# Performance work log

Measured on AMD Instinct MI355X. Metric: run time of the kernel, lower is better.

## Reference

```python
import jax, jax.numpy as jnp
import numpy as np
import math

B, S, D = 4, 2048, 1024
H = 1
HD = D // H  # head_dim == hidden_dim since num_heads=1 (required by source's phase_encoder Linear)
HALF = HD // 2
SYNC_LOSS_WEIGHT = 0.01


def setup_inputs() -> dict:
    key = jax.random.key(0)
    ks = jax.random.split(key, 11)
    wstd = 0.02
    inp = {
        "x": jax.random.normal(ks[0], (B, S, D), dtype=jnp.float32),
        "Wq": jax.random.normal(ks[1], (D, D), dtype=jnp.float32) * wstd,
        "bq": jnp.zeros((D,), jnp.float32),
        "Wk": jax.random.normal(ks[2], (D, D), dtype=jnp.float32) * wstd,
        "bk": jnp.zeros((D,), jnp.float32),
        "Wv": jax.random.normal(ks[3], (D, D), dtype=jnp.float32) * wstd,
        "bv": jnp.zeros((D,), jnp.float32),
        "Wp": jax.random.normal(ks[4], (D, D), dtype=jnp.float32) * wstd,
        "bp": jnp.zeros((D,), jnp.float32),
        "Wo": jax.random.normal(ks[5], (D, D), dtype=jnp.float32) * wstd,
        "bo": jnp.zeros((D,), jnp.float32),
        "bifurcation_param": jnp.asarray(1.0, jnp.float32),
        "phase_coupling": jnp.asarray(0.5, jnp.float32),
    }
    return inp


def _phase(t, Wp, bp):
    # t: [B,H,S,HD] -> instantaneous phase via angle(complex(first_half, second_half))
    pf = t @ Wp.T + bp
    re, im = pf[..., :HALF], pf[..., HALF:]
    return jnp.arctan2(im, re)  # [B,H,S,HALF]


def reference(x, Wq, bq, Wk, bk, Wv, bv, Wp, bp, Wo, bo, bifurcation_param, phase_coupling):
    b, s, d = x.shape
    Q = (x @ Wq.T + bq).reshape(b, s, H, HD).transpose(0, 2, 1, 3)  # [B,H,S,HD]
    K = (x @ Wk.T + bk).reshape(b, s, H, HD).transpose(0, 2, 1, 3)
    V = (x @ Wv.T + bv).reshape(b, s, H, HD).transpose(0, 2, 1, 3)

    scores = jnp.einsum("bhqd,bhkd->bhqk", Q, K) / math.sqrt(HD)

    pQ = _phase(Q, Wp, bp)
    pK = _phase(K, Wp, bp)
    # mean_d cos(pQ - pK) == (cos(pQ)@cos(pK)^T + sin(pQ)@sin(pK)^T) / HALF
    sync = (jnp.einsum("bhqd,bhkd->bhqk", jnp.cos(pQ), jnp.cos(pK))
            + jnp.einsum("bhqd,bhkd->bhqk", jnp.sin(pQ), jnp.sin(pK))) / HALF

    t = jnp.tanh(scores)
    bif = bifurcation_param * t * (1.0 - t)

    chaotic = scores + phase_coupling * sync + bif
    attn = jax.nn.softmax(chaotic, axis=-1)

    av = jnp.einsum("bhqk,bhkd->bhqd", attn, V)
    av = av.transpose(0, 2, 1, 3).reshape(b, s, d)
    out = av @ Wo.T + bo

    # torch.var default: unbiased (ddof=1), over last dim of sync
    sync_loss = SYNC_LOSS_WEIGHT * jnp.var(sync, axis=-1, ddof=1).mean()
    return out, sync_loss
```

## Files before the change

kernel.cpp:

```cpp
#include <hip/hip_runtime.h>
#include <hip/hip_bf16.h>
#include <math.h>

#define S_LEN 2048
#define D_MODEL 1024
#define N_BATCH 4
#define N_HALF 512

typedef unsigned short u16;
typedef __attribute__((ext_vector_type(8))) short bf16x8;
typedef __attribute__((ext_vector_type(4))) float f32x4;

__device__ inline u16 f2bf(float v) {
  __hip_bfloat16 h = __float2bfloat16(v);
  return *reinterpret_cast<u16*>(&h);
}
__device__ inline float bf2f(u16 u) {
  __hip_bfloat16 h = *reinterpret_cast<__hip_bfloat16*>(&u);
  return __bfloat162float(h);
}
__device__ inline void gl2lds16(const void* g, void* l) {
  __builtin_amdgcn_global_load_lds(
      (const __attribute__((address_space(1))) unsigned int*)g,
      (__attribute__((address_space(3))) unsigned int*)l, 16, 0, 0);
}
__device__ inline float fast_tanh(float x) {
  float e = __expf(2.0f * x);
  return 1.0f - 2.0f / (e + 1.0f);
}

__global__ __launch_bounds__(256)
void cast_bf4(const float* __restrict__ src, u16* __restrict__ dst, long long n4) {
  long long i = (long long)blockIdx.x * 256 + threadIdx.x;
  if (i >= n4) return;
  float4 v = ((const float4*)src)[i];
  ushort4 o;
  o.x = f2bf(v.x); o.y = f2bf(v.y); o.z = f2bf(v.z); o.w = f2bf(v.w);
  ((ushort4*)dst)[i] = o;
}
__global__ __launch_bounds__(256)
void cast_split(const float* __restrict__ src, u16* __restrict__ hi,
                u16* __restrict__ lo, long long n) {
  long long i = (long long)blockIdx.x * 256 + threadIdx.x;
  if (i < n) {
    float v = src[i];
    u16 h = f2bf(v);
    hi[i] = h;
    lo[i] = f2bf(v - bf2f(h));
  }
}
__global__ __launch_bounds__(256)
void transpose_split(const float* __restrict__ src, u16* __restrict__ hi,
                     u16* __restrict__ lo) {
  __shared__ float t[32][33];
  const int bx = blockIdx.x * 32;
  const int by = blockIdx.y * 32;
  const int c = threadIdx.x & 31;
  const int r0 = (threadIdx.x >> 5) * 4;
#pragma unroll
  for (int r = 0; r < 4; r++)
    t[r0 + r][c] = src[(long long)(by + r0 + r) * D_MODEL + bx + c];
  __syncthreads();
#pragma unroll
  for (int r = 0; r < 4; r++) {
    float v = t[c][r0 + r];
    long long idx = (long long)(bx + r0 + r) * D_MODEL + by + c;
    u16 h = f2bf(v);
    hi[idx] = h;
    lo[idx] = f2bf(v - bf2f(h));
  }
}
__global__ __launch_bounds__(256)
void zero_stats(float* __restrict__ p, int n) {
  int i = blockIdx.x * 256 + threadIdx.x;
  if (i < n) p[i] = 0.f;
}
__global__ __launch_bounds__(256)
void w2_bias(const float* __restrict__ Wo, const float* __restrict__ bv,
             float* __restrict__ w2b) {
  const int d = blockIdx.x;
  const int tid = threadIdx.x;
  float acc = 0.f;
  for (int j = tid; j < D_MODEL; j += 256)
    acc += Wo[(long long)d * D_MODEL + j] * bv[j];
#pragma unroll
  for (int m = 1; m < 64; m <<= 1) acc += __shfl_xor(acc, m);
  __shared__ float red[4];
  if ((tid & 63) == 0) red[tid >> 6] = acc;
  __syncthreads();
  if (tid == 0) w2b[d] = red[0] + red[1] + red[2] + red[3];
}


__global__ __launch_bounds__(256, 2)
void qk_fused(const u16* __restrict__ X, const u16* __restrict__ Wq,
              const u16* __restrict__ Wk,
              const float* __restrict__ bq, const float* __restrict__ bk,
              u16* __restrict__ Qo, u16* __restrict__ Ko) {
  __shared__ u16 Xs[128 * 64];
  __shared__ u16 Qs[128 * 64];
  __shared__ u16 Ks[128 * 64];
  const int tid  = threadIdx.x;
  const int wave = tid >> 6;
  const int lane = tid & 63;
  const int quad = lane >> 4;
  const int tc   = lane & 15;
  const int bm = blockIdx.y * 128;
  const int bn = blockIdx.x * 128;
  const int wm = (wave & 1) * 64;
  const int wn = (wave >> 1) * 64;

  f32x4 acc1[4][4], acc2[4][4];
#pragma unroll
  for (int i = 0; i < 4; i++)
#pragma unroll
    for (int j = 0; j < 4; j++) {
      acc1[i][j] = (f32x4){0.f, 0.f, 0.f, 0.f};
      acc2[i][j] = (f32x4){0.f, 0.f, 0.f, 0.f};
    }

  const int srow8 = lane >> 3;
  const int scol  = ((lane & 7) ^ srow8) * 8;
  const int srowb = wave * 32;
  const u16* gx = X  + (long long)(bm + srowb + srow8) * D_MODEL + scol;
  const u16* gq = Wq + (long long)(bn + srowb + srow8) * D_MODEL + scol;
  const u16* gk = Wk + (long long)(bn + srowb + srow8) * D_MODEL + scol;
  const int wb = srowb * 64;
  const long long r8 = 8LL * D_MODEL;
  const int swzA = tc & 7;

  for (int k0 = 0; k0 < D_MODEL; k0 += 64) {
#pragma unroll
    for (int c = 0; c < 4; c++) {
      gl2lds16(gx + c * r8, Xs + wb + c * 512);
      gl2lds16(gq + c * r8, Qs + wb + c * 512);
      gl2lds16(gk + c * r8, Ks + wb + c * 512);
    }
    gx += 64; gq += 64; gk += 64;
    __syncthreads();
    bf16x8 af[4][2], bq4[4][2], bk4[4][2];
#pragma unroll
    for (int i = 0; i < 4; i++) {
      const int ra = (wm + i * 16 + tc) * 64;
      const int rb = (wn + i * 16 + tc) * 64;
#pragma unroll
      for (int ks = 0; ks < 2; ks++) {
        const int co = ((ks * 4 + quad) ^ swzA) * 8;
        af[i][ks]  = *(const bf16x8*)(Xs + ra + co);
        bq4[i][ks] = *(const bf16x8*)(Qs + rb + co);
        bk4[i][ks] = *(const bf16x8*)(Ks + rb + co);
      }
    }
#pragma unroll
    for (int i = 0; i < 4; i++)
#pragma unroll
      for (int j = 0; j < 4; j++) {
        acc1[i][j] = __builtin_amdgcn_mfma_f32_16x16x32_bf16(af[i][0], bq4[j][0], acc1[i][j], 0, 0, 0);
        acc2[i][j] = __builtin_amdgcn_mfma_f32_16x16x32_bf16(af[i][0], bk4[j][0], acc2[i][j], 0, 0, 0);
        acc1[i][j] = __builtin_amdgcn_mfma_f32_16x16x32_bf16(af[i][1], bq4[j][1], acc1[i][j], 0, 0, 0);
        acc2[i][j] = __builtin_amdgcn_mfma_f32_16x16x32_bf16(af[i][1], bk4[j][1], acc2[i][j], 0, 0, 0);
      }
    __syncthreads();
  }

#pragma unroll
  for (int i = 0; i < 4; i++) {
    const int row0 = bm + wm + i * 16 + quad * 4;
#pragma unroll
    for (int j = 0; j < 4; j++) {
      const int col = bn + wn + j * 16 + tc;
#pragma unroll
      for (int r = 0; r < 4; r++) {
        long long idx = (long long)(row0 + r) * D_MODEL + col;
        Qo[idx] = f2bf(acc1[i][j][r] + bq[col]);
        Ko[idx] = f2bf(acc2[i][j][r] + bk[col]);
      }
    }
  }
}

__global__ __launch_bounds__(256, 2)
void pf_fused(const u16* __restrict__ Qb, const u16* __restrict__ Wp,
              const float* __restrict__ bp,
              u16* __restrict__ pfQ, u16* __restrict__ pfK,
              long long TDo) {
  __shared__ u16 Qs[128 * 64];
  __shared__ u16 Ks[128 * 64];
  __shared__ u16 Ws[128 * 64];
  const int tid  = threadIdx.x;
  const int wave = tid >> 6;
  const int lane = tid & 63;
  const int quad = lane >> 4;
  const int tc   = lane & 15;
  const int bm = blockIdx.y * 128;
  const int bn = blockIdx.x * 128;
  const int wm = (wave & 1) * 64;
  const int wn = (wave >> 1) * 64;

  f32x4 acc1[4][4], acc2[4][4];
#pragma unroll
  for (int i = 0; i < 4; i++)
#pragma unroll
    for (int j = 0; j < 4; j++) {
      acc1[i][j] = (f32x4){0.f, 0.f, 0.f, 0.f};
      acc2[i][j] = (f32x4){0.f, 0.f, 0.f, 0.f};
    }

  const int srow8 = lane >> 3;
  const int scol  = ((lane & 7) ^ srow8) * 8;
  const int srowb = wave * 32;
  const u16* gq = Qb + (long long)(bm + srowb + srow8) * D_MODEL + scol;
  const u16* gk = gq + TDo;
  const u16* gw = Wp + (long long)(bn + srowb + srow8) * D_MODEL + scol;
  const int wb = srowb * 64;
  const long long r8 = 8LL * D_MODEL;
  const int swzA = tc & 7;

  for (int k0 = 0; k0 < D_MODEL; k0 += 64) {
#pragma unroll
    for (int c = 0; c < 4; c++) {
      gl2lds16(gq + c * r8, Qs + wb + c * 512);
      gl2lds16(gk + c * r8, Ks + wb + c * 512);
      gl2lds16(gw + c * r8, Ws + wb + c * 512);
    }
    gq += 64; gk += 64; gw += 64;
    __syncthreads();
    bf16x8 aq[4][2], ak[4][2], bw[4][2];
#pragma unroll
    for (int i = 0; i < 4; i++) {
      const int ra = (wm + i * 16 + tc) * 64;
      const int rb = (wn + i * 16 + tc) * 64;
#pragma unroll
      for (int ks = 0; ks < 2; ks++) {
        const int co = ((ks * 4 + quad) ^ swzA) * 8;
        aq[i][ks] = *(const bf16x8*)(Qs + ra + co);
        ak[i][ks] = *(const bf16x8*)(Ks + ra + co);
        bw[i][ks] = *(const bf16x8*)(Ws + rb + co);
      }
    }
#pragma unroll
    for (int i = 0; i < 4; i++)
#pragma unroll
      for (int j = 0; j < 4; j++) {
        acc1[i][j] = __builtin_amdgcn_mfma_f32_16x16x32_bf16(aq[i][0], bw[j][0], acc1[i][j], 0, 0, 0);
        acc2[i][j] = __builtin_amdgcn_mfma_f32_16x16x32_bf16(ak[i][0], bw[j][0], acc2[i][j], 0, 0, 0);
        acc1[i][j] = __builtin_amdgcn_mfma_f32_16x16x32_bf16(aq[i][1], bw[j][1], acc1[i][j], 0, 0, 0);
        acc2[i][j] = __builtin_amdgcn_mfma_f32_16x16x32_bf16(ak[i][1], bw[j][1], acc2[i][j], 0, 0, 0);
      }
    __syncthreads();
  }

#pragma unroll
  for (int i = 0; i < 4; i++) {
    const int row0 = bm + wm + i * 16 + quad * 4;
#pragma unroll
    for (int j = 0; j < 4; j++) {
      const int col = bn + wn + j * 16 + tc;
#pragma unroll
      for (int r = 0; r < 4; r++) {
        long long idx = (long long)(row0 + r) * D_MODEL + col;
        float b = bp[col];
        pfQ[idx] = f2bf(acc1[i][j][r] + b);
        pfK[idx] = f2bf(acc2[i][j][r] + b);
      }
    }
  }
}

__global__ __launch_bounds__(256)
void mfma_gemm_out3(const u16* __restrict__ Ah, const u16* __restrict__ Al,
                    const u16* __restrict__ Bh, const u16* __restrict__ Bl,
                    const float* __restrict__ bias, float* __restrict__ C,
                    int N, int K) {
  __shared__ u16 Ash[128 * 64];
  __shared__ u16 Asl[128 * 64];
  __shared__ u16 Bsh[128 * 64];
  __shared__ u16 Bsl[128 * 64];
  const int tid  = threadIdx.x;
  const int wave = tid >> 6;
  const int lane = tid & 63;
  const int quad = lane >> 4;
  const int tc   = lane & 15;
  const int bm = blockIdx.y * 128;
  const int bn = blockIdx.x * 128;
  const int wm = (wave & 1) * 64;
  const int wn = (wave >> 1) * 64;

  f32x4 acc[4][4];
#pragma unroll
  for (int i = 0; i < 4; i++)
#pragma unroll
    for (int j = 0; j < 4; j++) acc[i][j] = (f32x4){0.f, 0.f, 0.f, 0.f};

  const int srow8 = lane >> 3;
  const int scol  = ((lane & 7) ^ srow8) * 8;
  const int srowb = wave * 32;
  long long aoff = (long long)(bm + srowb + srow8) * K + scol;
  long long boff = (long long)(bn + srowb + srow8) * K + scol;
  const u16 *gah = Ah + aoff, *gal = Al + aoff;
  const u16 *gbh = Bh + boff, *gbl = Bl + boff;
  const int wb = srowb * 64;
  const long long r8K = 8LL * K;
  const int swzA = tc & 7;

  for (int k0 = 0; k0 < K; k0 += 64) {
#pragma unroll
    for (int c = 0; c < 4; c++) {
      gl2lds16(gah + c * r8K, Ash + wb + c * 512);
      gl2lds16(gal + c * r8K, Asl + wb + c * 512);
      gl2lds16(gbh + c * r8K, Bsh + wb + c * 512);
      gl2lds16(gbl + c * r8K, Bsl + wb + c * 512);
    }
    gah += 64; gal += 64; gbh += 64; gbl += 64;
    __syncthreads();
    bf16x8 ah[4][2], al[4][2], bh[4][2], bl[4][2];
#pragma unroll
    for (int i = 0; i < 4; i++) {
      const int ra = (wm + i * 16 + tc) * 64;
      const int rb = (wn + i * 16 + tc) * 64;
#pragma unroll
      for (int ks = 0; ks < 2; ks++) {
        const int co = ((ks * 4 + quad) ^ swzA) * 8;
        ah[i][ks] = *(const bf16x8*)(Ash + ra + co);
        al[i][ks] = *(const bf16x8*)(Asl + ra + co);
        bh[i][ks] = *(const bf16x8*)(Bsh + rb + co);
        bl[i][ks] = *(const bf16x8*)(Bsl + rb + co);
      }
    }
#pragma unroll
    for (int i = 0; i < 4; i++)
#pragma unroll
      for (int j = 0; j < 4; j++) {
#pragma unroll
        for (int ks = 0; ks < 2; ks++) {
          acc[i][j] = __builtin_amdgcn_mfma_f32_16x16x32_bf16(ah[i][ks], bh[j][ks], acc[i][j], 0, 0, 0);
          acc[i][j] = __builtin_amdgcn_mfma_f32_16x16x32_bf16(ah[i][ks], bl[j][ks], acc[i][j], 0, 0, 0);
          acc[i][j] = __builtin_amdgcn_mfma_f32_16x16x32_bf16(al[i][ks], bh[j][ks], acc[i][j], 0, 0, 0);
        }
      }
    __syncthreads();
  }
#pragma unroll
  for (int i = 0; i < 4; i++) {
    const int row0 = bm + wm + i * 16 + quad * 4;
#pragma unroll
    for (int j = 0; j < 4; j++) {
      const int col = bn + wn + j * 16 + tc;
      float b = bias ? bias[col] : 0.f;
#pragma unroll
      for (int r = 0; r < 4; r++)
        C[(long long)(row0 + r) * N + col] = acc[i][j][r] + b;
    }
  }
}

__global__ __launch_bounds__(256)
void vwt_kernel(const u16* __restrict__ W2h, const u16* __restrict__ W2l,
                const u16* __restrict__ X, const float* __restrict__ w2b,
                u16* __restrict__ Ch, u16* __restrict__ Cl,
                long long sB, long long sC) {
  __shared__ u16 Ah[128 * 64];
  __shared__ u16 Al[128 * 64];
  __shared__ u16 Bs[128 * 64];
  const int tid  = threadIdx.x;
  const int wave = tid >> 6;
  const int lane = tid & 63;
  const int quad = lane >> 4;
  const int tc   = lane & 15;
  const int bm = blockIdx.y * 128;
  const int bn = blockIdx.x * 128;
  const long long z = blockIdx.z;
  const int wm = (wave & 1) * 64;
  const int wn = (wave >> 1) * 64;

  f32x4 acc[4][4];
#pragma unroll
  for (int i = 0; i < 4; i++)
#pragma unroll
    for (int j = 0; j < 4; j++) acc[i][j] = (f32x4){0.f, 0.f, 0.f, 0.f};

  const int srow8 = lane >> 3;
  const int scol  = ((lane & 7) ^ srow8) * 8;
  const int srowb = wave * 32;
  const long long aoff = (long long)(bm + srowb + srow8) * D_MODEL + scol;
  const u16* gah = W2h + aoff;
  const u16* gal = W2l + aoff;
  const u16* gb  = X + z * sB + (long long)(bn + srowb + srow8) * D_MODEL + scol;
  const int wb = srowb * 64;
  const long long r8 = 8LL * D_MODEL;
  const int swzA = tc & 7;

  for (int k0 = 0; k0 < D_MODEL; k0 += 64) {
#pragma unroll
    for (int c = 0; c < 4; c++) {
      gl2lds16(gah + c * r8, Ah + wb + c * 512);
      gl2lds16(gal + c * r8, Al + wb + c * 512);
      gl2lds16(gb  + c * r8, Bs + wb + c * 512);
    }
    gah += 64; gal += 64; gb += 64;
    __syncthreads();
    bf16x8 ah4[4][2], al4[4][2], bx[4][2];
#pragma unroll
    for (int i = 0; i < 4; i++) {
      const int ra = (wm + i * 16 + tc) * 64;
      const int rb = (wn + i * 16 + tc) * 64;
#pragma unroll
      for (int ks = 0; ks < 2; ks++) {
        const int co = ((ks * 4 + quad) ^ swzA) * 8;
        ah4[i][ks] = *(const bf16x8*)(Ah + ra + co);
        al4[i][ks] = *(const bf16x8*)(Al + ra + co);
        bx[i][ks]  = *(const bf16x8*)(Bs + rb + co);
      }
    }
#pragma unroll
    for (int i = 0; i < 4; i++)
#pragma unroll
      for (int j = 0; j < 4; j++) {
        acc[i][j] = __builtin_amdgcn_mfma_f32_16x16x32_bf16(ah4[i][0], bx[j][0], acc[i][j], 0, 0, 0);
        acc[i][j] = __builtin_amdgcn_mfma_f32_16x16x32_bf16(al4[i][0], bx[j][0], acc[i][j], 0, 0, 0);
        acc[i][j] = __builtin_amdgcn_mfma_f32_16x16x32_bf16(ah4[i][1], bx[j][1], acc[i][j], 0, 0, 0);
        acc[i][j] = __builtin_amdgcn_mfma_f32_16x16x32_bf16(al4[i][1], bx[j][1], acc[i][j], 0, 0, 0);
      }
    __syncthreads();
  }

  u16* Chz = Ch + z * sC;
  u16* Clz = Cl + z * sC;
#pragma unroll
  for (int i = 0; i < 4; i++) {
    const int row0 = bm + wm + i * 16 + quad * 4;
#pragma unroll
    for (int j = 0; j < 4; j++) {
      const int col = bn + wn + j * 16 + tc;
#pragma unroll
      for (int r = 0; r < 4; r++) {
        float v = acc[i][j][r] + w2b[row0 + r];
        long long idx = (long long)(row0 + r) * S_LEN + col;
        u16 h = f2bf(v);
        Chz[idx] = h;
        Clz[idx] = f2bf(v - bf2f(h));
      }
    }
  }
}

__global__ __launch_bounds__(256)
void gemm_bsplit(const u16* __restrict__ A,
                 const u16* __restrict__ Bh, const u16* __restrict__ Bl,
                 const float* __restrict__ bias, float* __restrict__ C,
                 int N, int K, long long sA, long long sB, long long sC) {
  __shared__ u16 As[128 * 64];
  __shared__ u16 Bsh[128 * 64];
  __shared__ u16 Bsl[128 * 64];
  const int tid  = threadIdx.x;
  const int wave = tid >> 6;
  const int lane = tid & 63;
  const int quad = lane >> 4;
  const int tc   = lane & 15;
  const int bm = blockIdx.y * 128;
  const int bn = blockIdx.x * 128;
  const long long z = blockIdx.z;
  const int wm = (wave & 1) * 64;
  const int wn = (wave >> 1) * 64;

  f32x4 acc[4][4];
#pragma unroll
  for (int i = 0; i < 4; i++)
#pragma unroll
    for (int j = 0; j < 4; j++) acc[i][j] = (f32x4){0.f, 0.f, 0.f, 0.f};

  const int srow8 = lane >> 3;
  const int scol  = ((lane & 7) ^ srow8) * 8;
  const int srowb = wave * 32;
  const long long boff = (long long)(bn + srowb + srow8) * K + scol;
  const u16* ga  = A + z * sA + (long long)(bm + srowb + srow8) * K + scol;
  const u16* gbh = Bh + z * sB + boff;
  const u16* gbl = Bl + z * sB + boff;
  const int wb = srowb * 64;
  const long long r8K = 8LL * K;
  const int swzA = tc & 7;

  for (int k0 = 0; k0 < K; k0 += 64) {
#pragma unroll
    for (int c = 0; c < 4; c++) {
      gl2lds16(ga  + c * r8K, As  + wb + c * 512);
      gl2lds16(gbh + c * r8K, Bsh + wb + c * 512);
      gl2lds16(gbl + c * r8K, Bsl + wb + c * 512);
    }
    ga += 64; gbh += 64; gbl += 64;
    __syncthreads();
    bf16x8 af[4][2], bh[4][2], bl[4][2];
#pragma unroll
    for (int i = 0; i < 4; i++) {
      const int ra = (wm + i * 16 + tc) * 64;
      const int rb = (wn + i * 16 + tc) * 64;
#pragma unroll
      for (int ks = 0; ks < 2; ks++) {
        const int co = ((ks * 4 + quad) ^ swzA) * 8;
        af[i][ks] = *(const bf16x8*)(As  + ra + co);
        bh[i][ks] = *(const bf16x8*)(Bsh + rb + co);
        bl[i][ks] = *(const bf16x8*)(Bsl + rb + co);
      }
    }
#pragma unroll
    for (int i = 0; i < 4; i++)
#pragma unroll
      for (int j = 0; j < 4; j++) {
        acc[i][j] = __builtin_amdgcn_mfma_f32_16x16x32_bf16(af[i][0], bh[j][0], acc[i][j], 0, 0, 0);
        acc[i][j] = __builtin_amdgcn_mfma_f32_16x16x32_bf16(af[i][0], bl[j][0], acc[i][j], 0, 0, 0);
        acc[i][j] = __builtin_amdgcn_mfma_f32_16x16x32_bf16(af[i][1], bh[j][1], acc[i][j], 0, 0, 0);
        acc[i][j] = __builtin_amdgcn_mfma_f32_16x16x32_bf16(af[i][1], bl[j][1], acc[i][j], 0, 0, 0);
      }
    __syncthreads();
  }

  float* Cz = C + z * sC;
#pragma unroll
  for (int i = 0; i < 4; i++) {
    const int row0 = bm + wm + i * 16 + quad * 4;
#pragma unroll
    for (int j = 0; j < 4; j++) {
      const int col = bn + wn + j * 16 + tc;
#pragma unroll
      for (int r = 0; r < 4; r++)
        Cz[(long long)(row0 + r) * N + col] = acc[i][j][r] + bias[col];
    }
  }
}

__global__ __launch_bounds__(256, 2)
void chaotic_fused(const u16* __restrict__ Q, const u16* __restrict__ Kt,
                   const u16* __restrict__ Uq, const u16* __restrict__ Uk,
                   float* __restrict__ Cc,
                   float* __restrict__ ssum, float* __restrict__ ssq,
                   const float* __restrict__ bifp, const float* __restrict__ pcp) {
  __shared__ u16 Qs[128 * 64];
  __shared__ u16 Ks[128 * 64];
  __shared__ u16 Us[128 * 64];
  __shared__ u16 Ws[128 * 64];
  const int tid  = threadIdx.x;
  const int wave = tid >> 6;
  const int lane = tid & 63;
  const int quad = lane >> 4;
  const int tc   = lane & 15;
  const int bm = blockIdx.y * 128;
  const int bn = blockIdx.x * 128;
  const long long z = blockIdx.z;
  const long long sQ = (long long)S_LEN * D_MODEL;
  const int wm = (wave & 1) * 64;
  const int wn = (wave >> 1) * 64;

  f32x4 acc1[4][4], acc2[4][4];
#pragma unroll
  for (int i = 0; i < 4; i++)
#pragma unroll
    for (int j = 0; j < 4; j++) {
      acc1[i][j] = (f32x4){0.f, 0.f, 0.f, 0.f};
      acc2[i][j] = (f32x4){0.f, 0.f, 0.f, 0.f};
    }

  const int srow8  = lane >> 3;
  const int scol   = ((lane & 7) ^ srow8) * 8;
  const int srowb  = wave * 32;
  const u16* gq = Q  + z * sQ + (long long)(bm + srowb + srow8) * D_MODEL + scol;
  const u16* gk = Kt + z * sQ + (long long)(bn + srowb + srow8) * D_MODEL + scol;
  const u16* gu = Uq + z * sQ + (long long)(bm + srowb + srow8) * D_MODEL + scol;
  const u16* gw = Uk + z * sQ + (long long)(bn + srowb + srow8) * D_MODEL + scol;
  const int wb = srowb * 64;
  const long long r8 = 8LL * D_MODEL;

  const int swzA = tc & 7;

  for (int k0 = 0; k0 < D_MODEL; k0 += 64) {
#pragma unroll
    for (int c = 0; c < 4; c++) {
      gl2lds16(gq + c * r8, Qs + wb + c * 512);
      gl2lds16(gk + c * r8, Ks + wb + c * 512);
      gl2lds16(gu + c * r8, Us + wb + c * 512);
      gl2lds16(gw + c * r8, Ws + wb + c * 512);
    }
    gq += 64; gk += 64; gu += 64; gw += 64;
    __syncthreads();
    {
      bf16x8 af[4][2], bg[4][2];
#pragma unroll
      for (int i = 0; i < 4; i++) {
        const int ra = (wm + i * 16 + tc) * 64;
        const int rb = (wn + i * 16 + tc) * 64;
#pragma unroll
        for (int ks = 0; ks < 2; ks++) {
          const int co = ((ks * 4 + quad) ^ swzA) * 8;
          af[i][ks] = *(const bf16x8*)(Qs + ra + co);
          bg[i][ks] = *(const bf16x8*)(Ks + rb + co);
        }
      }
#pragma unroll
      for (int i = 0; i < 4; i++)
#pragma unroll
        for (int j = 0; j < 4; j++) {
          acc1[i][j] = __builtin_amdgcn_mfma_f32_16x16x32_bf16(af[i][0], bg[j][0], acc1[i][j], 0, 0, 0);
          acc1[i][j] = __builtin_amdgcn_mfma_f32_16x16x32_bf16(af[i][1], bg[j][1], acc1[i][j], 0, 0, 0);
        }
    }
    {
      bf16x8 cf[4][2], dg[4][2];
#pragma unroll
      for (int i = 0; i < 4; i++) {
        const int ra = (wm + i * 16 + tc) * 64;
        const int rb = (wn + i * 16 + tc) * 64;
#pragma unroll
        for (int ks = 0; ks < 2; ks++) {
          const int co = ((ks * 4 + quad) ^ swzA) * 8;
          cf[i][ks] = *(const bf16x8*)(Us + ra + co);
          dg[i][ks] = *(const bf16x8*)(Ws + rb + co);
        }
      }
#pragma unroll
      for (int i = 0; i < 4; i++)
#pragma unroll
        for (int j = 0; j < 4; j++) {
          acc2[i][j] = __builtin_amdgcn_mfma_f32_16x16x32_bf16(cf[i][0], dg[j][0], acc2[i][j], 0, 0, 0);
          acc2[i][j] = __builtin_amdgcn_mfma_f32_16x16x32_bf16(cf[i][1], dg[j][1], acc2[i][j], 0, 0, 0);
        }
    }
    __syncthreads();
  }

  const float bif = *bifp;
  const float pc  = *pcp;
  float rsum[4][4], rsq[4][4];
#pragma unroll
  for (int i = 0; i < 4; i++)
#pragma unroll
    for (int r = 0; r < 4; r++) { rsum[i][r] = 0.f; rsq[i][r] = 0.f; }

  float* C = Cc + z * (long long)S_LEN * S_LEN;
#pragma unroll
  for (int i = 0; i < 4; i++) {
    const int row0 = bm + wm + i * 16 + quad * 4;
#pragma unroll
    for (int j = 0; j < 4; j++) {
      const int col = bn + wn + j * 16 + tc;
#pragma unroll
      for (int r = 0; r < 4; r++) {
        float sc = acc1[i][j][r] * 0.03125f;
        float sy = acc2[i][j][r] * (1.0f / 512.0f);
        float t  = fast_tanh(sc);
        C[(long long)(row0 + r) * S_LEN + col] = sc + pc * sy + bif * t * (1.0f - t);
        rsum[i][r] += sy;
        rsq[i][r]  += sy * sy;
      }
    }
  }
#pragma unroll
  for (int m = 1; m < 16; m <<= 1) {
#pragma unroll
    for (int i = 0; i < 4; i++)
#pragma unroll
      for (int r = 0; r < 4; r++) {
        rsum[i][r] += __shfl_xor(rsum[i][r], m);
        rsq[i][r]  += __shfl_xor(rsq[i][r], m);
      }
  }
  if (tc == 0) {
#pragma unroll
    for (int i = 0; i < 4; i++)
#pragma unroll
      for (int r = 0; r < 4; r++) {
        long long rr = z * S_LEN + bm + wm + i * 16 + quad * 4 + r;
        atomicAdd(&ssum[rr], rsum[i][r]);
        atomicAdd(&ssq[rr],  rsq[i][r]);
      }
  }
}

__global__ __launch_bounds__(256)
void phase_norm_bf(u16* __restrict__ U, long long n_rows) {
  long long idx = (long long)blockIdx.x * 256 + threadIdx.x;
  if (idx >= n_rows * 64) return;
  long long row = idx >> 6;
  int j0 = (int)(idx & 63) * 8;
  u16* p = U + row * D_MODEL + j0;
  bf16x8 re8 = *(const bf16x8*)p;
  bf16x8 im8 = *(const bf16x8*)(p + N_HALF);
  bf16x8 ro, io;
#pragma unroll
  for (int i = 0; i < 8; i++) {
    float re = bf2f((u16)re8[i]);
    float im = bf2f((u16)im8[i]);
    float n2 = re * re + im * im;
    float cr = 1.f, sr = 0.f;
    if (n2 > 0.f) {
      float inv = 1.0f / sqrtf(n2);
      cr = re * inv; sr = im * inv;
    }
    ro[i] = (short)f2bf(cr);
    io[i] = (short)f2bf(sr);
  }
  *(bf16x8*)p = ro;
  *(bf16x8*)(p + N_HALF) = io;
}

__global__ __launch_bounds__(256)
void softmax_bf(const float* __restrict__ Cc, u16* __restrict__ P) {
  const long long row = (long long)blockIdx.y * S_LEN + blockIdx.x;
  const float* p = Cc + row * S_LEN;
  u16* q = P + row * S_LEN;
  const int tid = threadIdx.x;
  float v[8];
  float m = -3.402823466e+38f;
#pragma unroll
  for (int i = 0; i < 8; i++) { v[i] = p[tid + i * 256]; m = fmaxf(m, v[i]); }
#pragma unroll
  for (int mask = 1; mask < 64; mask <<= 1) m = fmaxf(m, __shfl_xor(m, mask));
  __shared__ float red[8];
  if ((tid & 63) == 0) red[tid >> 6] = m;
  __syncthreads();
  m = fmaxf(fmaxf(red[0], red[1]), fmaxf(red[2], red[3]));
  float s = 0.f;
#pragma unroll
  for (int i = 0; i < 8; i++) { v[i] = __expf(v[i] - m); s += v[i]; }
#pragma unroll
  for (int mask = 1; mask < 64; mask <<= 1) s += __shfl_xor(s, mask);
  __syncthreads();
  if ((tid & 63) == 0) red[4 + (tid >> 6)] = s;
  __syncthreads();
  s = red[4] + red[5] + red[6] + red[7];
  float inv = 1.0f / s;
#pragma unroll
  for (int i = 0; i < 8; i++) q[tid + i * 256] = f2bf(v[i] * inv);
}

__global__ __launch_bounds__(1024)
void syncloss_kernel(const float* __restrict__ ssum, const float* __restrict__ ssq,
                     float* __restrict__ out) {
  const int tid = threadIdx.x;
  float acc = 0.f;
  for (int r = tid; r < N_BATCH * S_LEN; r += 1024) {
    float su = ssum[r], sq = ssq[r];
    acc += (sq - su * su * (1.0f / 2048.0f)) * (1.0f / 2047.0f);
  }
#pragma unroll
  for (int mask = 1; mask < 64; mask <<= 1) acc += __shfl_xor(acc, mask);
  __shared__ float red[16];
  if ((tid & 63) == 0) red[tid >> 6] = acc;
  __syncthreads();
  if (tid == 0) {
    float t = 0.f;
#pragma unroll
    for (int k = 0; k < 16; k++) t += red[k];
    out[0] = 0.01f * (t / (float)(N_BATCH * S_LEN));
  }
}

extern "C" void kernel_launch(void* const* d_in, const int* in_sizes, int n_in,
                              void* d_out, int out_size, void* d_ws, size_t ws_size,
                              hipStream_t stream) {
  const float* x    = (const float*)d_in[0];
  const float* Wq   = (const float*)d_in[1];
  const float* bq   = (const float*)d_in[2];
  const float* Wk   = (const float*)d_in[3];
  const float* bk   = (const float*)d_in[4];
  const float* Wv   = (const float*)d_in[5];
  const float* bv   = (const float*)d_in[6];
  const float* Wp   = (const float*)d_in[7];
  const float* bp   = (const float*)d_in[8];
  const float* Wo   = (const float*)d_in[9];
  const float* bo   = (const float*)d_in[10];
  const float* bifp = (const float*)d_in[11];
  const float* pcp  = (const float*)d_in[12];
  float* out = (float*)d_out;

  const long long NROW = (long long)N_BATCH * S_LEN;
  const long long TD   = NROW * D_MODEL;
  const long long WSZ  = (long long)D_MODEL * D_MODEL;

  u16* xbf   = (u16*)d_ws;
  u16* wqb   = xbf + TD;
  u16* wkb   = wqb + WSZ;
  u16* wpb   = wkb + WSZ;
  u16* woh   = wpb + WSZ;
  u16* wol   = woh + WSZ;
  u16* wvth  = wol + WSZ;
  u16* wvtl  = wvth + WSZ;
  u16* w2h   = wvtl + WSZ;
  u16* w2l   = w2h + WSZ;
  float* W2f = (float*)(w2l + WSZ);
  float* w2b = W2f + WSZ;
  u16* Qbf   = (u16*)(w2b + D_MODEL);
  u16* Kbf   = Qbf + TD;
  u16* pfQ   = Kbf + TD;
  u16* pfK   = pfQ + TD;
  float* Cc  = (float*)(pfK + TD);
  float* ssum = Cc + (long long)N_BATCH * S_LEN * S_LEN;
  float* ssq  = ssum + NROW;
  u16* attn = Qbf;
  u16* vwh  = pfQ;
  u16* vwl  = pfK;

  dim3 blk(256);
  const long long sQ = (long long)S_LEN * D_MODEL;
  const long long sS = (long long)S_LEN * S_LEN;

  cast_bf4<<<(int)(TD / 4 / 256), blk, 0, stream>>>(x, xbf, TD / 4);
  cast_bf4<<<(int)(WSZ / 4 / 256), blk, 0, stream>>>(Wq, wqb, WSZ / 4);
  cast_bf4<<<(int)(WSZ / 4 / 256), blk, 0, stream>>>(Wk, wkb, WSZ / 4);
  cast_bf4<<<(int)(WSZ / 4 / 256), blk, 0, stream>>>(Wp, wpb, WSZ / 4);
  cast_split<<<(int)(WSZ / 256), blk, 0, stream>>>(Wo, woh, wol, WSZ);
  transpose_split<<<dim3(32, 32), blk, 0, stream>>>(Wv, wvth, wvtl);
  mfma_gemm_out3<<<dim3(8, 8, 1), blk, 0, stream>>>(
      woh, wol, wvth, wvtl, nullptr, W2f, D_MODEL, D_MODEL);
  cast_split<<<(int)(WSZ / 256), blk, 0, stream>>>(W2f, w2h, w2l, WSZ);
  w2_bias<<<D_MODEL, blk, 0, stream>>>(Wo, bv, w2b);

  qk_fused<<<dim3(8, 64), blk, 0, stream>>>(xbf, wqb, wkb, bq, bk, Qbf, Kbf);
  pf_fused<<<dim3(8, 64), blk, 0, stream>>>(Qbf, wpb, bp, pfQ, pfK, TD);
  phase_norm_bf<<<(int)(2 * NROW * 64 / 256), blk, 0, stream>>>(pfQ, 2 * NROW);
  zero_stats<<<(int)((2 * NROW + 255) / 256), blk, 0, stream>>>(ssum, (int)(2 * NROW));

  chaotic_fused<<<dim3(16, 16, N_BATCH), blk, 0, stream>>>(
      Qbf, Kbf, pfQ, pfK, Cc, ssum, ssq, bifp, pcp);
  vwt_kernel<<<dim3(16, 8, N_BATCH), blk, 0, stream>>>(
      w2h, w2l, xbf, w2b, vwh, vwl, sQ, sQ);
  softmax_bf<<<dim3(S_LEN, N_BATCH), blk, 0, stream>>>(Cc, attn);
  gemm_bsplit<<<dim3(8, 16, N_BATCH), blk, 0, stream>>>(
      attn, vwh, vwl, bo, out,
      D_MODEL, S_LEN, sS, sQ, sQ);
  syncloss_kernel<<<1, 1024, 0, stream>>>(ssum, ssq, out + TD);
}
```

Before: 488.3 us.

## Fuse phase normalization into phase GEMM epilogue and merge cast kernels

```diff
diff --git a/kernel.cpp b/kernel.cpp
--- a/kernel.cpp
+++ b/kernel.cpp
@@ -29,14 +29,27 @@
   return 1.0f - 2.0f / (e + 1.0f);
 }
 
+#define N0_X   (2097152LL)
+#define NW_W   (262144LL)
 __global__ __launch_bounds__(256)
-void cast_bf4(const float* __restrict__ src, u16* __restrict__ dst, long long n4) {
+void cast_bf4_multi(const float* __restrict__ sx, u16* __restrict__ dx,
+                    const float* __restrict__ s1, u16* __restrict__ d1,
+                    const float* __restrict__ s2, u16* __restrict__ d2,
+                    const float* __restrict__ s3, u16* __restrict__ d3) {
   long long i = (long long)blockIdx.x * 256 + threadIdx.x;
-  if (i >= n4) return;
-  float4 v = ((const float4*)src)[i];
+  const float* s; u16* d; long long off;
+  if (i < N0_X) { s = sx; d = dx; off = i; }
+  else {
+    long long k = i - N0_X;
+    int w = (int)(k >> 18);
+    off = k & (NW_W - 1);
+    s = (w == 0) ? s1 : (w == 1) ? s2 : s3;
+    d = (w == 0) ? d1 : (w == 1) ? d2 : d3;
+  }
+  float4 v = ((const float4*)s)[off];
   ushort4 o;
   o.x = f2bf(v.x); o.y = f2bf(v.y); o.z = f2bf(v.z); o.w = f2bf(v.w);
-  ((ushort4*)dst)[i] = o;
+  ((ushort4*)d)[off] = o;
 }
 __global__ __launch_bounds__(256)
 void cast_split(const float* __restrict__ src, u16* __restrict__ hi,
@@ -69,11 +82,6 @@
     hi[idx] = h;
     lo[idx] = f2bf(v - bf2f(h));
   }
-}
-__global__ __launch_bounds__(256)
-void zero_stats(float* __restrict__ p, int n) {
-  int i = blockIdx.x * 256 + threadIdx.x;
-  if (i < n) p[i] = 0.f;
 }
 __global__ __launch_bounds__(256)
 void w2_bias(const float* __restrict__ Wo, const float* __restrict__ bv,
@@ -184,18 +192,19 @@
               const float* __restrict__ bp,
               u16* __restrict__ pfQ, u16* __restrict__ pfK,
               long long TDo) {
-  __shared__ u16 Qs[128 * 64];
-  __shared__ u16 Ks[128 * 64];
-  __shared__ u16 Ws[128 * 64];
+  __shared__ u16 lds_all[3 * 128 * 64];
+  u16* Qs = lds_all;
+  u16* Ks = lds_all + 128 * 64;
+  u16* Ws = lds_all + 2 * 128 * 64;
   const int tid  = threadIdx.x;
   const int wave = tid >> 6;
   const int lane = tid & 63;
   const int quad = lane >> 4;
   const int tc   = lane & 15;
   const int bm = blockIdx.y * 128;
-  const int bn = blockIdx.x * 128;
+  const int bn = blockIdx.x * 64;
   const int wm = (wave & 1) * 64;
-  const int wn = (wave >> 1) * 64;
+  const int grp = wave >> 1;
 
   f32x4 acc1[4][4], acc2[4][4];
 #pragma unroll
@@ -211,7 +220,7 @@
   const int srowb = wave * 32;
   const u16* gq = Qb + (long long)(bm + srowb + srow8) * D_MODEL + scol;
   const u16* gk = gq + TDo;
-  const u16* gw = Wp + (long long)(bn + srowb + srow8) * D_MODEL + scol;
+  const u16* gw = Wp + (long long)(bn + srowb + srow8 + ((wave & 2) ? 448 : 0)) * D_MODEL + scol;
   const int wb = srowb * 64;
   const long long r8 = 8LL * D_MODEL;
   const int swzA = tc & 7;
@@ -226,6 +235,7 @@
     gq += 64; gk += 64; gw += 64;
     __syncthreads();
     bf16x8 aq[4][2], ak[4][2], bw[4][2];
+    const int wn = grp * 64;
 #pragma unroll
     for (int i = 0; i < 4; i++) {
       const int ra = (wm + i * 16 + tc) * 64;
@@ -250,19 +260,45 @@
     __syncthreads();
   }
 
-#pragma unroll
-  for (int i = 0; i < 4; i++) {
-    const int row0 = bm + wm + i * 16 + quad * 4;
-#pragma unroll
-    for (int j = 0; j < 4; j++) {
-      const int col = bn + wn + j * 16 + tc;
-#pragma unroll
-      for (int r = 0; r < 4; r++) {
-        long long idx = (long long)(row0 + r) * D_MODEL + col;
-        float b = bp[col];
-        pfQ[idx] = f2bf(acc1[i][j][r] + b);
-        pfK[idx] = f2bf(acc2[i][j][r] + b);
-      }
+  float* ex = (float*)lds_all;
+  const long long colbase = (long long)bn + (long long)grp * 512;
+#pragma unroll
+  for (int o = 0; o < 2; o++) {
+    u16* Ou = o ? pfK : pfQ;
+#pragma unroll
+    for (int half = 0; half < 2; half++) {
+      int cnt = 0;
+#pragma unroll
+      for (int i = 2 * half; i < 2 * half + 2; i++)
+#pragma unroll
+        for (int j = 0; j < 4; j++) {
+          f32x4 v = o ? acc2[i][j] : acc1[i][j];
+          float b = bp[colbase + j * 16 + tc];
+          v[0] += b; v[1] += b; v[2] += b; v[3] += b;
+          *(f32x4*)(ex + wave * 2048 + cnt * 256 + lane * 4) = v;
+          cnt++;
+        }
+      __syncthreads();
+      cnt = 0;
+#pragma unroll
+      for (int i = 2 * half; i < 2 * half + 2; i++)
+#pragma unroll
+        for (int j = 0; j < 4; j++) {
+          f32x4 own = *(const f32x4*)(ex + wave * 2048 + cnt * 256 + lane * 4);
+          f32x4 oth = *(const f32x4*)(ex + (wave ^ 2) * 2048 + cnt * 256 + lane * 4);
+          const int row0 = bm + wm + i * 16 + quad * 4;
+          const long long col = colbase + j * 16 + tc;
+#pragma unroll
+          for (int r = 0; r < 4; r++) {
+            float a = own[r], p = oth[r];
+            float n2 = a * a + p * p;
+            float outv = (grp == 0) ? 1.f : 0.f;
+            if (n2 > 0.f) outv = a * (1.0f / sqrtf(n2));
+            Ou[(long long)(row0 + r) * D_MODEL + col] = f2bf(outv);
+          }
+          cnt++;
+        }
+      __syncthreads();
     }
   }
 }
@@ -672,33 +708,6 @@
         atomicAdd(&ssq[rr],  rsq[i][r]);
       }
   }
-}
-
-__global__ __launch_bounds__(256)
-void phase_norm_bf(u16* __restrict__ U, long long n_rows) {
-  long long idx = (long long)blockIdx.x * 256 + threadIdx.x;
-  if (idx >= n_rows * 64) return;
-  long long row = idx >> 6;
-  int j0 = (int)(idx & 63) * 8;
-  u16* p = U + row * D_MODEL + j0;
-  bf16x8 re8 = *(const bf16x8*)p;
-  bf16x8 im8 = *(const bf16x8*)(p + N_HALF);
-  bf16x8 ro, io;
-#pragma unroll
-  for (int i = 0; i < 8; i++) {
-    float re = bf2f((u16)re8[i]);
-    float im = bf2f((u16)im8[i]);
-    float n2 = re * re + im * im;
-    float cr = 1.f, sr = 0.f;
-    if (n2 > 0.f) {
-      float inv = 1.0f / sqrtf(n2);
-      cr = re * inv; sr = im * inv;
-    }
-    ro[i] = (short)f2bf(cr);
-    io[i] = (short)f2bf(sr);
-  }
-  *(bf16x8*)p = ro;
-  *(bf16x8*)(p + N_HALF) = io;
 }
 
 __global__ __launch_bounds__(256)
@@ -802,10 +811,7 @@
   const long long sQ = (long long)S_LEN * D_MODEL;
   const long long sS = (long long)S_LEN * S_LEN;
 
-  cast_bf4<<<(int)(TD / 4 / 256), blk, 0, stream>>>(x, xbf, TD / 4);
-  cast_bf4<<<(int)(WSZ / 4 / 256), blk, 0, stream>>>(Wq, wqb, WSZ / 4);
-  cast_bf4<<<(int)(WSZ / 4 / 256), blk, 0, stream>>>(Wk, wkb, WSZ / 4);
-  cast_bf4<<<(int)(WSZ / 4 / 256), blk, 0, stream>>>(Wp, wpb, WSZ / 4);
+  cast_bf4_multi<<<11264, blk, 0, stream>>>(x, xbf, Wq, wqb, Wk, wkb, Wp, wpb);
   cast_split<<<(int)(WSZ / 256), blk, 0, stream>>>(Wo, woh, wol, WSZ);
   transpose_split<<<dim3(32, 32), blk, 0, stream>>>(Wv, wvth, wvtl);
   mfma_gemm_out3<<<dim3(8, 8, 1), blk, 0, stream>>>(
@@ -815,8 +821,7 @@
 
   qk_fused<<<dim3(8, 64), blk, 0, stream>>>(xbf, wqb, wkb, bq, bk, Qbf, Kbf);
   pf_fused<<<dim3(8, 64), blk, 0, stream>>>(Qbf, wpb, bp, pfQ, pfK, TD);
-  phase_norm_bf<<<(int)(2 * NROW * 64 / 256), blk, 0, stream>>>(pfQ, 2 * NROW);
-  zero_stats<<<(int)((2 * NROW + 255) / 256), blk, 0, stream>>>(ssum, (int)(2 * NROW));
+  hipMemsetAsync(ssum, 0, (size_t)(2 * NROW) * sizeof(float), stream);
 
   chaotic_fused<<<dim3(16, 16, N_BATCH), blk, 0, stream>>>(
       Qbf, Kbf, pfQ, pfK, Cc, ssum, ssq, bifp, pcp);
```

New measurement: 487.4 us. About the same (-0.2%).
